# Optimization experiments

Measured on AMD Instinct MI355X. Metric: run time of the kernel, lower is better.

Reference implementation:

```python
import jax, jax.numpy as jnp
import numpy as np

STRIDE, PAD, DIL = 1, 1, 1


def setup_inputs() -> dict:
    key = jax.random.key(0)
    k1, k2, k3, k4, k5 = jax.random.split(key, 5)
    N, Cin, H, W = 8, 256, 64, 64
    Cout, K = 256, 3
    x = jax.random.normal(k1, (N, Cin, H, W), dtype=jnp.float32)
    offset = jax.random.normal(k2, (N, 2 * K * K, H, W), dtype=jnp.float32)
    mask = jax.random.uniform(k3, (N, K * K, H, W), dtype=jnp.float32)
    weight = jax.random.normal(k4, (Cout, Cin, K, K), dtype=jnp.float32) * 0.02
    bias = jax.random.normal(k5, (Cout,), dtype=jnp.float32)
    return {"x": x, "offset": offset, "mask": mask, "weight": weight, "bias": bias}


def _gather(im_flat, idx):
    # im_flat: (N, Goff, Cg, H*W); idx: (N, Goff, KK, Ho, Wo) int32
    # -> (N, Goff, Cg, KK, Ho, Wo)
    f = lambda imf, ix: imf[:, ix]
    return jax.vmap(jax.vmap(f))(im_flat, idx)


def _deform_conv2d(x, offset, mask, weight, bias):
    N, Cin, H, W = x.shape
    Cout, Cin_g, Kh, Kw = weight.shape
    KK = Kh * Kw
    Goff = offset.shape[1] // (2 * KK)
    Ho = (H + 2 * PAD - (DIL * (Kh - 1) + 1)) // STRIDE + 1
    Wo = (W + 2 * PAD - (DIL * (Kw - 1) + 1)) // STRIDE + 1

    # base sampling grid per kernel tap: (KK, Ho, Wo)
    py = (jnp.arange(Kh)[:, None] * DIL + jnp.arange(Ho)[None, :] * STRIDE - PAD).astype(jnp.float32)
    px = (jnp.arange(Kw)[:, None] * DIL + jnp.arange(Wo)[None, :] * STRIDE - PAD).astype(jnp.float32)
    y_base = jnp.broadcast_to(py[:, None, :, None], (Kh, Kw, Ho, Wo)).reshape(KK, Ho, Wo)
    x_base = jnp.broadcast_to(px[None, :, None, :], (Kh, Kw, Ho, Wo)).reshape(KK, Ho, Wo)

    off = offset.reshape(N, Goff, KK, 2, Ho, Wo)  # [...,0]=dy, [...,1]=dx
    ys = y_base[None, None] + off[:, :, :, 0]  # (N, Goff, KK, Ho, Wo)
    xs = x_base[None, None] + off[:, :, :, 1]

    Cg = Cin // Goff
    im_flat = x.reshape(N, Goff, Cg, H * W)

    y0 = jnp.floor(ys)
    x0 = jnp.floor(xs)
    acc = jnp.zeros((N, Goff, Cg, KK, Ho, Wo), dtype=x.dtype)
    for dy in (0.0, 1.0):
        for dx in (0.0, 1.0):
            yi = y0 + dy
            xi = x0 + dx
            wgt = (1.0 - jnp.abs(ys - yi)) * (1.0 - jnp.abs(xs - xi))
            valid = (yi >= 0) & (yi < H) & (xi >= 0) & (xi < W)
            idx = (jnp.clip(yi, 0, H - 1) * W + jnp.clip(xi, 0, W - 1)).astype(jnp.int32)
            g = _gather(im_flat, idx)  # (N,Goff,Cg,KK,Ho,Wo)
            acc = acc + g * (wgt * valid.astype(x.dtype))[:, :, None]

    m = mask.reshape(N, Goff, KK, Ho, Wo)
    sampled = acc * m[:, :, None]  # DCNv2 modulation

    # grouped conv accumulate as GEMM over (Cin_g*KK)
    gw = Cin // Cin_g
    cols = sampled.reshape(N, gw, Cin_g * KK, Ho * Wo)
    wflat = weight.reshape(gw, Cout // gw, Cin_g * KK)
    out = jnp.einsum('goc,ngcl->ngol', wflat, cols).reshape(N, Cout, Ho, Wo)
    return out + bias[None, :, None, None]


def reference(x, offset, mask, weight, bias):
    return _deform_conv2d(x, offset, mask, weight, bias)
```

## Files before the change

### kernel.cpp

```cpp
#include <hip/hip_runtime.h>
#include <stdint.h>

typedef unsigned int u32;
typedef unsigned short u16;
typedef float f32x4 __attribute__((ext_vector_type(4)));
typedef __fp16 h16x2 __attribute__((ext_vector_type(2)));
typedef _Float16 f16x8 __attribute__((ext_vector_type(8)));
typedef float f4u __attribute__((ext_vector_type(4), aligned(4)));

#define NB   8
#define CIN  256
#define HH   64
#define WW   64
#define HW   4096
#define COUT 256
#define NPX  128
#define BSTR 264

__device__ __forceinline__ u32 pkh(float lo, float hi) {
  h16x2 h = __builtin_amdgcn_cvt_pkrtz(lo, hi);
  return __builtin_bit_cast(u32, h);
}
union HU { u32 u; h16x2 h; };

__global__ __launch_bounds__(256) void prep_all(const float* __restrict__ x,
                                                const float* __restrict__ wgt,
                                                u32* __restrict__ xT,
                                                u32* __restrict__ W2f32) {
  int b = blockIdx.x;
  int t = threadIdx.x;
  if (b < 512) {
    __shared__ u32 tile[64][129];
    int n = b >> 6, hw0 = (b & 63) << 6;
    int hw4 = (t & 15) << 2;
    int cp0 = t >> 4;
    const float* xb = x + (size_t)n * CIN * HW + hw0 + hw4;
#pragma unroll
    for (int it = 0; it < 8; ++it) {
      int cp = (it << 4) + cp0;
      int c = cp << 1;
      f4u v0 = *(const f4u*)(xb + (size_t)c * HW);
      f4u v1 = *(const f4u*)(xb + (size_t)(c + 1) * HW);
      tile[hw4 + 0][cp] = pkh(v0.x, v1.x);
      tile[hw4 + 1][cp] = pkh(v0.y, v1.y);
      tile[hw4 + 2][cp] = pkh(v0.z, v1.z);
      tile[hw4 + 3][cp] = pkh(v0.w, v1.w);
    }
    __syncthreads();
    u32* outp = xT + ((size_t)(n * HW + hw0)) * 128;
    int cp = t & 127, hb = t >> 7;
#pragma unroll
    for (int it = 0; it < 32; ++it) {
      int hwl = (it << 1) + hb;
      outp[(size_t)hwl * 128 + cp] = tile[hwl][cp];
    }
  } else {
    int tt = (b - 512) * 256 + t;
    int cp = tt & 127, co = tt >> 7;
    int c = cp << 1;
    const float* p = wgt + ((size_t)co * CIN + c) * 9;
    f4u q0 = *(const f4u*)(p + 0);
    f4u q1 = *(const f4u*)(p + 4);
    f4u q2 = *(const f4u*)(p + 8);
    f4u q3 = *(const f4u*)(p + 12);
    float e16 = p[16], e17 = p[17];
    float a0[9], a1[9];
    a0[0]=q0.x; a0[1]=q0.y; a0[2]=q0.z; a0[3]=q0.w;
    a0[4]=q1.x; a0[5]=q1.y; a0[6]=q1.z; a0[7]=q1.w; a0[8]=q2.x;
    a1[0]=q2.y; a1[1]=q2.z; a1[2]=q2.w;
    a1[3]=q3.x; a1[4]=q3.y; a1[5]=q3.z; a1[6]=q3.w; a1[7]=e16; a1[8]=e17;
    int cc = c >> 5;
    int j = (c >> 1) & 3;
    int lane = (co & 15) | (((c >> 3) & 3) << 4);
    int tile_ = ((co >> 6) << 2) | ((co >> 4) & 3);
#pragma unroll
    for (int kk = 0; kk < 9; ++kk) {
      int frag = (kk * 8 + cc) * 16 + tile_;
      W2f32[(size_t)frag * 256 + lane * 4 + j] = pkh(a0[kk], a1[kk]);
    }
  }
}

__global__ __launch_bounds__(1024, 4) void dcn_main(
    const float* __restrict__ offset, const float* __restrict__ mask,
    const float* __restrict__ bias, const u16* __restrict__ xT,
    const u16* __restrict__ W2f, float* __restrict__ out) {
  __shared__ __align__(16) u16 Bs[2][NPX * BSTR];
  __shared__ __align__(8)  uint2 swl[1152];
  __shared__ __align__(8)  ushort4 sol[1152];

  int bid = blockIdx.x;
  int n = bid & 7;
  int hp = bid >> 3;
  int t = threadIdx.x;
  int lane = t & 63;
  int w = t >> 6;

  for (int i = t; i < 1152; i += 1024) {
    int kk = i >> 7, p = i & 127;
    int ky = kk / 3, kx = kk - ky * 3;
    int sp = (hp << 7) + p;
    int ho = (hp << 1) + (p >> 6);
    float dy = offset[(((size_t)n * 18 + kk * 2 + 0) << 12) + sp];
    float dx = offset[(((size_t)n * 18 + kk * 2 + 1) << 12) + sp];
    float m  = mask  [(((size_t)n * 9  + kk) << 12) + sp];
    float ys = (float)(ky + ho - 1) + dy;
    float xs = (float)(kx + (p & 63) - 1) + dx;
    float y0f = floorf(ys), x0f = floorf(xs);
    float fy = ys - y0f, fx = xs - x0f;
    int y0 = (int)y0f, x0 = (int)x0f;
    int y1 = y0 + 1, x1 = x0 + 1;
    float vy0 = (y0 >= 0 && y0 < HH) ? 1.f : 0.f;
    float vy1 = (y1 >= 0 && y1 < HH) ? 1.f : 0.f;
    float vx0 = (x0 >= 0 && x0 < WW) ? 1.f : 0.f;
    float vx1 = (x1 >= 0 && x1 < WW) ? 1.f : 0.f;
    float w0 = (1.f - fy) * (1.f - fx) * m * vy0 * vx0;
    float w1 = (1.f - fy) * fx * m * vy0 * vx1;
    float w2 = fy * (1.f - fx) * m * vy1 * vx0;
    float w3 = fy * fx * m * vy1 * vx1;
    int iy0 = min(max(y0, 0), HH - 1), iy1 = min(max(y1, 0), HH - 1);
    int ix0 = min(max(x0, 0), WW - 1), ix1 = min(max(x1, 0), WW - 1);
    ushort4 pv;
    pv.x = (u16)((iy0 << 6) + ix0);
    pv.y = (u16)((iy0 << 6) + ix1);
    pv.z = (u16)((iy1 << 6) + ix0);
    pv.w = (u16)((iy1 << 6) + ix1);
    swl[i] = make_uint2(pkh(w0, w1), pkh(w2, w3));
    sol[i] = pv;
  }
  __syncthreads();

  f32x4 acc[2][8];
#pragma unroll
  for (int a = 0; a < 2; ++a)
#pragma unroll
    for (int b2 = 0; b2 < 8; ++b2) acc[a][b2] = {0.f, 0.f, 0.f, 0.f};

  const char* xTn = (const char*)xT + ((size_t)n * HW << 9);
  int ml = lane & 15, q = lane >> 4;
  int hw32 = t >> 5;
  int l32 = t & 31;
  int strip = w & 7, pr = w >> 3;
  int tile0 = ((strip >> 1) << 2) + ((strip & 1) << 1);
  const char* bch = xTn + (l32 << 4);

#define CMB(G, WT) do {                                                \
    float wt = (WT);                                                   \
    HU h0, h1, h2, h3;                                                 \
    h0.u = (G).x; h1.u = (G).y; h2.u = (G).z; h3.u = (G).w;            \
    s0 = __builtin_fmaf((float)h0.h.x, wt, s0);                        \
    s1 = __builtin_fmaf((float)h0.h.y, wt, s1);                        \
    s2 = __builtin_fmaf((float)h1.h.x, wt, s2);                        \
    s3 = __builtin_fmaf((float)h1.h.y, wt, s3);                        \
    s4 = __builtin_fmaf((float)h2.h.x, wt, s4);                        \
    s5 = __builtin_fmaf((float)h2.h.y, wt, s5);                        \
    s6 = __builtin_fmaf((float)h3.h.x, wt, s6);                        \
    s7 = __builtin_fmaf((float)h3.h.y, wt, s7);                        \
  } while (0)

  auto build0 = [&](int g) {
    int px = (g << 5) + hw32;
    uint2 wu = swl[px];
    ushort4 pv = sol[px];
    HU ha, hb; ha.u = wu.x; hb.u = wu.y;
    uint4 G0 = *(const uint4*)(bch + ((int)pv.x << 9));
    uint4 G1 = *(const uint4*)(bch + ((int)pv.y << 9));
    uint4 G2 = *(const uint4*)(bch + ((int)pv.z << 9));
    uint4 G3 = *(const uint4*)(bch + ((int)pv.w << 9));
    float s0=0.f,s1=0.f,s2=0.f,s3=0.f,s4=0.f,s5=0.f,s6=0.f,s7=0.f;
    CMB(G0, (float)ha.h.x);
    CMB(G1, (float)ha.h.y);
    CMB(G2, (float)hb.h.x);
    CMB(G3, (float)hb.h.y);
    uint4 pkd;
    pkd.x = pkh(s0, s1); pkd.y = pkh(s2, s3);
    pkd.z = pkh(s4, s5); pkd.w = pkh(s6, s7);
    *(uint4*)((char*)&Bs[0][0] + px * (BSTR * 2) + (l32 << 4)) = pkd;
  };

  auto af_load = [&](int fidx, int mt) {
    return *(const f16x8*)(W2f + (((size_t)((fidx << 4) + tile0 + mt)) << 9) +
                           (lane << 3));
  };

#pragma unroll
  for (int g = 0; g < 4; ++g) build0(g);
  __syncthreads();

#pragma unroll 1
  for (int kk = 0; kk < 9; ++kk) {
    int cur = kk & 1;
    char* Bw = (char*)&Bs[cur ^ 1][0];
    const char* Br = (const char*)&Bs[cur][0];
    int fbase = kk << 3;
#pragma unroll
    for (int g = 0; g < 4; ++g) {
      int px = (g << 5) + hw32;
      uint4 G0, G1, G2, G3;
      if (kk < 8) {
        ushort4 pv = sol[((kk + 1) << 7) + px];
        G0 = *(const uint4*)(bch + ((int)pv.x << 9));
        G1 = *(const uint4*)(bch + ((int)pv.y << 9));
        G2 = *(const uint4*)(bch + ((int)pv.z << 9));
        G3 = *(const uint4*)(bch + ((int)pv.w << 9));
      }
      {
        int cc = (g << 1) | pr;
        f16x8 af0 = af_load(fbase + cc, 0);
        f16x8 af1 = af_load(fbase + cc, 1);
        f16x8 bf[4];
#pragma unroll
        for (int half = 0; half < 2; ++half) {
#pragma unroll
          for (int j = 0; j < 4; ++j)
            bf[j] = *(const f16x8*)(Br +
                    ((((half << 2) + j) << 4) + ml) * (BSTR * 2) +
                    (cc << 6) + (q << 4));
#pragma unroll
          for (int j = 0; j < 4; ++j)
            acc[0][(half << 2) + j] = __builtin_amdgcn_mfma_f32_16x16x32_f16(
                af0, bf[j], acc[0][(half << 2) + j], 0, 0, 0);
#pragma unroll
          for (int j = 0; j < 4; ++j)
            acc[1][(half << 2) + j] = __builtin_amdgcn_mfma_f32_16x16x32_f16(
                af1, bf[j], acc[1][(half << 2) + j], 0, 0, 0);
        }
      }
      if (kk < 8) {
        uint2 wu = swl[((kk + 1) << 7) + px];
        HU ha, hb; ha.u = wu.x; hb.u = wu.y;
        float s0=0.f,s1=0.f,s2=0.f,s3=0.f,s4=0.f,s5=0.f,s6=0.f,s7=0.f;
        CMB(G0, (float)ha.h.x);
        CMB(G1, (float)ha.h.y);
        CMB(G2, (float)hb.h.x);
        CMB(G3, (float)hb.h.y);
        uint4 pkd;
        pkd.x = pkh(s0, s1); pkd.y = pkh(s2, s3);
        pkd.z = pkh(s4, s5); pkd.w = pkh(s6, s7);
        *(uint4*)(Bw + px * (BSTR * 2) + (l32 << 4)) = pkd;
      }
    }
    __syncthreads();
  }

  float* PS = (float*)&Bs[0][0];
  float* P = PS + strip * 4224 + lane * 66;
  if (pr) {
#pragma unroll
    for (int mt = 0; mt < 2; ++mt)
#pragma unroll
      for (int nt = 0; nt < 8; ++nt)
#pragma unroll
        for (int r = 0; r < 4; ++r)
          P[((mt << 3) + nt) * 4 + r] = acc[mt][nt][r];
  }
  __syncthreads();
  if (!pr) {
    size_t ob = (size_t)n * COUT * HW + ((size_t)hp << 7);
#pragma unroll
    for (int mt = 0; mt < 2; ++mt) {
#pragma unroll
      for (int r = 0; r < 4; ++r) {
        int co = (strip << 5) + (mt << 4) + (q << 2) + r;
        float bv = bias[co];
#pragma unroll
        for (int nt = 0; nt < 8; ++nt) {
          int px = (nt << 4) + ml;
          out[ob + (size_t)co * HW + px] =
              acc[mt][nt][r] + P[((mt << 3) + nt) * 4 + r] + bv;
        }
      }
    }
  }
}

extern "C" void kernel_launch(void* const* d_in, const int* in_sizes, int n_in,
                              void* d_out, int out_size, void* d_ws, size_t ws_size,
                              hipStream_t stream) {
  const float* x      = (const float*)d_in[0];
  const float* offset = (const float*)d_in[1];
  const float* mask   = (const float*)d_in[2];
  const float* weight = (const float*)d_in[3];
  const float* bias   = (const float*)d_in[4];
  float* out = (float*)d_out;

  u16* xT  = (u16*)d_ws;
  u16* W2f = (u16*)((char*)d_ws + (size_t)NB * HW * CIN * 2);

  prep_all<<<640, 256, 0, stream>>>(x, weight, (u32*)xT, (u32*)W2f);
  dcn_main<<<256, 1024, 0, stream>>>(offset, mask, bias, xT, W2f, out);
}
```

Measured before the change: 143.7 us.

## Retile MFMA work by output pixels, prefetch weight fragments, use packed fp16 bilinear math

```diff
diff --git a/kernel.cpp b/kernel.cpp
--- a/kernel.cpp
+++ b/kernel.cpp
@@ -130,61 +130,66 @@
   }
   __syncthreads();
 
-  f32x4 acc[2][8];
-#pragma unroll
-  for (int a = 0; a < 2; ++a)
-#pragma unroll
-    for (int b2 = 0; b2 < 8; ++b2) acc[a][b2] = {0.f, 0.f, 0.f, 0.f};
+  f32x4 acc[4][2];
+#pragma unroll
+  for (int a = 0; a < 4; ++a)
+#pragma unroll
+    for (int b2 = 0; b2 < 2; ++b2) acc[a][b2] = {0.f, 0.f, 0.f, 0.f};
 
   const char* xTn = (const char*)xT + ((size_t)n * HW << 9);
   int ml = lane & 15, q = lane >> 4;
   int hw32 = t >> 5;
   int l32 = t & 31;
-  int strip = w & 7, pr = w >> 3;
-  int tile0 = ((strip >> 1) << 2) + ((strip & 1) << 1);
+  int strip = w & 3;
+  int pq = w >> 2;
+  int tile0 = strip << 2;
   const char* bch = xTn + (l32 << 4);
 
-#define CMB(G, WT) do {                                                \
-    float wt = (WT);                                                   \
-    HU h0, h1, h2, h3;                                                 \
-    h0.u = (G).x; h1.u = (G).y; h2.u = (G).z; h3.u = (G).w;            \
-    s0 = __builtin_fmaf((float)h0.h.x, wt, s0);                        \
-    s1 = __builtin_fmaf((float)h0.h.y, wt, s1);                        \
-    s2 = __builtin_fmaf((float)h1.h.x, wt, s2);                        \
-    s3 = __builtin_fmaf((float)h1.h.y, wt, s3);                        \
-    s4 = __builtin_fmaf((float)h2.h.x, wt, s4);                        \
-    s5 = __builtin_fmaf((float)h2.h.y, wt, s5);                        \
-    s6 = __builtin_fmaf((float)h3.h.x, wt, s6);                        \
-    s7 = __builtin_fmaf((float)h3.h.y, wt, s7);                        \
+#define PKC(G, WD) do {                                                \
+    HU a0, a1, a2, a3;                                                 \
+    a0.u = (G).x; a1.u = (G).y; a2.u = (G).z; a3.u = (G).w;            \
+    s0 = a0.h * (WD) + s0;                                             \
+    s1 = a1.h * (WD) + s1;                                             \
+    s2 = a2.h * (WD) + s2;                                             \
+    s3 = a3.h * (WD) + s3;                                             \
   } while (0)
 
   auto build0 = [&](int g) {
     int px = (g << 5) + hw32;
     uint2 wu = swl[px];
     ushort4 pv = sol[px];
-    HU ha, hb; ha.u = wu.x; hb.u = wu.y;
+    HU ua, ub; ua.u = wu.x; ub.u = wu.y;
+    h16x2 w0d = __builtin_shufflevector(ua.h, ua.h, 0, 0);
+    h16x2 w1d = __builtin_shufflevector(ua.h, ua.h, 1, 1);
+    h16x2 w2d = __builtin_shufflevector(ub.h, ub.h, 0, 0);
+    h16x2 w3d = __builtin_shufflevector(ub.h, ub.h, 1, 1);
     uint4 G0 = *(const uint4*)(bch + ((int)pv.x << 9));
     uint4 G1 = *(const uint4*)(bch + ((int)pv.y << 9));
     uint4 G2 = *(const uint4*)(bch + ((int)pv.z << 9));
     uint4 G3 = *(const uint4*)(bch + ((int)pv.w << 9));
-    float s0=0.f,s1=0.f,s2=0.f,s3=0.f,s4=0.f,s5=0.f,s6=0.f,s7=0.f;
-    CMB(G0, (float)ha.h.x);
-    CMB(G1, (float)ha.h.y);
-    CMB(G2, (float)hb.h.x);
-    CMB(G3, (float)hb.h.y);
+    h16x2 s0 = {0.f16, 0.f16}, s1 = s0, s2 = s0, s3 = s0;
+    PKC(G0, w0d);
+    PKC(G1, w1d);
+    PKC(G2, w2d);
+    PKC(G3, w3d);
     uint4 pkd;
-    pkd.x = pkh(s0, s1); pkd.y = pkh(s2, s3);
-    pkd.z = pkh(s4, s5); pkd.w = pkh(s6, s7);
+    pkd.x = __builtin_bit_cast(u32, s0); pkd.y = __builtin_bit_cast(u32, s1);
+    pkd.z = __builtin_bit_cast(u32, s2); pkd.w = __builtin_bit_cast(u32, s3);
     *(uint4*)((char*)&Bs[0][0] + px * (BSTR * 2) + (l32 << 4)) = pkd;
   };
 
-  auto af_load = [&](int fidx, int mt) {
-    return *(const f16x8*)(W2f + (((size_t)((fidx << 4) + tile0 + mt)) << 9) +
-                           (lane << 3));
+  auto af_load4 = [&](int fidx, f16x8* dst) {
+#pragma unroll
+    for (int mt = 0; mt < 4; ++mt)
+      dst[mt] = *(const f16x8*)(W2f +
+                (((size_t)((fidx << 4) + tile0 + mt)) << 9) + (lane << 3));
   };
 
 #pragma unroll
   for (int g = 0; g < 4; ++g) build0(g);
+
+  f16x8 afr[2][4];
+  af_load4(0, afr[0]);
   __syncthreads();
 
 #pragma unroll 1
@@ -204,71 +209,57 @@
         G2 = *(const uint4*)(bch + ((int)pv.z << 9));
         G3 = *(const uint4*)(bch + ((int)pv.w << 9));
       }
-      {
-        int cc = (g << 1) | pr;
-        f16x8 af0 = af_load(fbase + cc, 0);
-        f16x8 af1 = af_load(fbase + cc, 1);
-        f16x8 bf[4];
-#pragma unroll
-        for (int half = 0; half < 2; ++half) {
-#pragma unroll
-          for (int j = 0; j < 4; ++j)
-            bf[j] = *(const f16x8*)(Br +
-                    ((((half << 2) + j) << 4) + ml) * (BSTR * 2) +
-                    (cc << 6) + (q << 4));
-#pragma unroll
-          for (int j = 0; j < 4; ++j)
-            acc[0][(half << 2) + j] = __builtin_amdgcn_mfma_f32_16x16x32_f16(
-                af0, bf[j], acc[0][(half << 2) + j], 0, 0, 0);
-#pragma unroll
-          for (int j = 0; j < 4; ++j)
-            acc[1][(half << 2) + j] = __builtin_amdgcn_mfma_f32_16x16x32_f16(
-                af1, bf[j], acc[1][(half << 2) + j], 0, 0, 0);
-        }
+#pragma unroll
+      for (int c2 = 0; c2 < 2; ++c2) {
+        int cc = (g << 1) | c2;
+        int fidx = fbase + cc;
+        int nf = fidx + 1; if (nf > 71) nf = 71;
+        af_load4(nf, afr[(cc + 1) & 1]);
+        f16x8 bf[2];
+#pragma unroll
+        for (int nt = 0; nt < 2; ++nt)
+          bf[nt] = *(const f16x8*)(Br +
+                   ((pq << 5) + (nt << 4) + ml) * (BSTR * 2) +
+                   (cc << 6) + (q << 4));
+#pragma unroll
+        for (int mt = 0; mt < 4; ++mt)
+#pragma unroll
+          for (int nt = 0; nt < 2; ++nt)
+            acc[mt][nt] = __builtin_amdgcn_mfma_f32_16x16x32_f16(
+                afr[cc & 1][mt], bf[nt], acc[mt][nt], 0, 0, 0);
       }
       if (kk < 8) {
         uint2 wu = swl[((kk + 1) << 7) + px];
-        HU ha, hb; ha.u = wu.x; hb.u = wu.y;
-        float s0=0.f,s1=0.f,s2=0.f,s3=0.f,s4=0.f,s5=0.f,s6=0.f,s7=0.f;
-        CMB(G0, (float)ha.h.x);
-        CMB(G1, (float)ha.h.y);
-        CMB(G2, (float)hb.h.x);
-        CMB(G3, (float)hb.h.y);
+        HU ua, ub; ua.u = wu.x; ub.u = wu.y;
+        h16x2 w0d = __builtin_shufflevector(ua.h, ua.h, 0, 0);
+        h16x2 w1d = __builtin_shufflevector(ua.h, ua.h, 1, 1);
+        h16x2 w2d = __builtin_shufflevector(ub.h, ub.h, 0, 0);
+        h16x2 w3d = __builtin_shufflevector(ub.h, ub.h, 1, 1);
+        h16x2 s0 = {0.f16, 0.f16}, s1 = s0, s2 = s0, s3 = s0;
+        PKC(G0, w0d);
+        PKC(G1, w1d);
+        PKC(G2, w2d);
+        PKC(G3, w3d);
         uint4 pkd;
-        pkd.x = pkh(s0, s1); pkd.y = pkh(s2, s3);
-        pkd.z = pkh(s4, s5); pkd.w = pkh(s6, s7);
+        pkd.x = __builtin_bit_cast(u32, s0); pkd.y = __builtin_bit_cast(u32, s1);
+        pkd.z = __builtin_bit_cast(u32, s2); pkd.w = __builtin_bit_cast(u32, s3);
         *(uint4*)(Bw + px * (BSTR * 2) + (l32 << 4)) = pkd;
       }
     }
     __syncthreads();
   }
 
-  float* PS = (float*)&Bs[0][0];
-  float* P = PS + strip * 4224 + lane * 66;
-  if (pr) {
-#pragma unroll
-    for (int mt = 0; mt < 2; ++mt)
-#pragma unroll
-      for (int nt = 0; nt < 8; ++nt)
-#pragma unroll
-        for (int r = 0; r < 4; ++r)
-          P[((mt << 3) + nt) * 4 + r] = acc[mt][nt][r];
-  }
-  __syncthreads();
-  if (!pr) {
-    size_t ob = (size_t)n * COUT * HW + ((size_t)hp << 7);
-#pragma unroll
-    for (int mt = 0; mt < 2; ++mt) {
-#pragma unroll
-      for (int r = 0; r < 4; ++r) {
-        int co = (strip << 5) + (mt << 4) + (q << 2) + r;
-        float bv = bias[co];
-#pragma unroll
-        for (int nt = 0; nt < 8; ++nt) {
-          int px = (nt << 4) + ml;
-          out[ob + (size_t)co * HW + px] =
-              acc[mt][nt][r] + P[((mt << 3) + nt) * 4 + r] + bv;
-        }
+  size_t ob = (size_t)n * COUT * HW + ((size_t)hp << 7);
+#pragma unroll
+  for (int mt = 0; mt < 4; ++mt) {
+#pragma unroll
+    for (int r = 0; r < 4; ++r) {
+      int co = ((tile0 + mt) << 4) + (q << 2) + r;
+      float bv = bias[co];
+#pragma unroll
+      for (int nt = 0; nt < 2; ++nt) {
+        int px = (pq << 5) + (nt << 4) + ml;
+        out[ob + (size_t)co * HW + px] = acc[mt][nt][r] + bv;
       }
     }
   }
```

After: 153.9 us. 7.1% more time.
